# Optimization experiments

Measured on AMD Instinct MI355X. Metric: run time of the kernel, lower is better.

Reference implementation:

```python
import jax, jax.numpy as jnp
import numpy as np

B, N1, N2 = 8, 2048, 2048


def setup_inputs() -> dict:
    key = jax.random.key(0)
    k1, k2 = jax.random.split(key)
    pc_gen = jax.random.normal(k1, (B, N1, 3), dtype=jnp.float32)
    pc_gt = jax.random.normal(k2, (B, N2, 3), dtype=jnp.float32)
    return {"pc_gen": pc_gen, "pc_gt": pc_gt}


def _approx_match(d2, n, m):
    """Faithful JAX port of Fan et al. approxmatch.cu iterative OT matching.
    d2: [B, n, m] squared pairwise distances. Returns match matrix [B, n, m]."""
    b = d2.shape[0]
    factorl = max(n, m) / n  # row capacity
    factorr = max(n, m) / m  # column capacity
    remainl0 = jnp.full((b, n), factorl, dtype=d2.dtype)
    remainr0 = jnp.full((b, m), factorr, dtype=d2.dtype)
    match0 = jnp.zeros_like(d2)
    # levels: j = 7 .. -1 -> -4^j, then final pass with level = 0 (j == -2 case)
    levels = jnp.asarray([-(4.0 ** j) for j in range(7, -2, -1)] + [0.0],
                         dtype=d2.dtype)

    def step(carry, level):
        match, remainl, remainr = carry
        w = jnp.exp(level * d2) * remainr[:, None, :]            # [b,n,m]
        w = w * (remainl / (w.sum(-1) + 1e-9))[:, :, None]       # row-normalize, scale by remainl
        colsum = w.sum(1)                                        # [b,m]
        ratio = jnp.minimum(remainr / (colsum + 1e-9), 1.0)      # column saturation ratio
        w = w * ratio[:, None, :]
        match = match + w
        remainl = jnp.maximum(remainl - w.sum(-1), 0.0)
        remainr = jnp.maximum(remainr - colsum * ratio, 0.0)
        return (match, remainl, remainr), None

    (match, _, _), _ = jax.lax.scan(step, (match0, remainl0, remainr0), levels)
    return match


def reference(pc_gen, pc_gt):
    n, m = pc_gen.shape[1], pc_gt.shape[1]
    diff = pc_gen[:, :, None, :] - pc_gt[:, None, :, :]          # [B,n,m,3]
    d2 = jnp.sum(diff * diff, axis=-1)                           # [B,n,m]
    match = jax.lax.stop_gradient(_approx_match(d2, n, m))
    # matchcost: sum of match-weighted Euclidean distances, per batch
    dist = jnp.sum(match * jnp.sqrt(jnp.maximum(d2, 1e-20)), axis=(1, 2))  # [B]
    emd_loss = (dist / n).mean()
    return emd_loss
```

## Files before the change

kernel.cpp:

```cpp
#include <hip/hip_runtime.h>
#include <math.h>

#define BATCH 8
#define NPTS 2048
#define MPTS 2048
#define TPB 256
#define RPB 16
#define KC 8
#define RPR 2
#define NRND (RPB/RPR)
#define CHUNKS (NPTS/RPB)
#define NBLK (BATCH*CHUNKS)

__device__ float g_remainl[BATCH*NPTS];
__device__ float g_s[BATCH*NPTS];
__device__ float g_rbuf[2][BATCH*MPTS];
__device__ float g_cbuf[3][BATCH*MPTS];
__device__ float g_cost;

#if __has_builtin(__builtin_amdgcn_exp2f)
#define EXP2(x) __builtin_amdgcn_exp2f(x)
#else
#define EXP2(x) exp2f(x)
#endif
#if __has_builtin(__builtin_amdgcn_sqrtf)
#define FSQRT(x) __builtin_amdgcn_sqrtf(x)
#else
#define FSQRT(x) sqrtf(x)
#endif
#if __has_builtin(__builtin_amdgcn_rcpf)
#define RCP(x) __builtin_amdgcn_rcpf(x)
#else
#define RCP(x) (1.0f/(x))
#endif

#define D2(rd, k) fmaf(rd.x, cx[k], fmaf(rd.y, cy[k],                      \
                   fmaf(rd.z, cz[k], rd.w + rc2[k])))

__global__ __launch_bounds__(256) void k_init() {
  const int i = blockIdx.x*256 + threadIdx.x;
  g_cbuf[0][i] = 0.f;
  g_cbuf[1][i] = 0.f;
  g_rbuf[0][i] = 1.f;
  if (i == 0) g_cost = 0.f;
}

__global__ __launch_bounds__(TPB) void k_a0(const float* __restrict__ gen,
                                            const float* __restrict__ gt,
                                            float c1) {
  const int blk = blockIdx.x, b = blk >> 7, chunk = blk & (CHUNKS-1);
  const int t = threadIdx.x, wave = t >> 6, lane = t & 63;
  const int rowbase = b*NPTS + chunk*RPB;
  __shared__ float4 rowdat[RPB];
  __shared__ float2 red[2][4];
  __shared__ float  cred[4];
  float cx[KC], cy[KC], cz[KC], rc2[KC];
  #pragma unroll
  for (int k = 0; k < KC; ++k) {
    const int gi = (b*MPTS + t + TPB*k)*3;
    cx[k] = gt[gi]; cy[k] = gt[gi+1]; cz[k] = gt[gi+2];
    rc2[k] = cx[k]*cx[k] + cy[k]*cy[k] + cz[k]*cz[k];
  }
  if (t < RPB) {
    const int gi = (rowbase + t)*3;
    const float px = gen[gi], py = gen[gi+1], pz = gen[gi+2];
    rowdat[t] = make_float4(-2.f*px, -2.f*py, -2.f*pz, px*px+py*py+pz*pz);
    g_remainl[rowbase + t] = 1.0f;
  }
  __syncthreads();
  float colacc[KC];
  #pragma unroll
  for (int k = 0; k < KC; ++k) colacc[k] = 0.f;
  #pragma unroll 1
  for (int rr = 0; rr < NRND; ++rr) {
    const int buf = rr & 1;
    const float4 rd0 = rowdat[RPR*rr+0];
    const float4 rd1 = rowdat[RPR*rr+1];
    float w0[KC], w1[KC];
    float s1a = 0.f, s1b = 0.f;
    #pragma unroll
    for (int k = 0; k < KC; ++k) {
      const float ea = EXP2(c1*D2(rd0, k));
      const float eb = EXP2(c1*D2(rd1, k));
      w0[k] = ea; s1a += ea;
      w1[k] = eb; s1b += eb;
    }
    #pragma unroll
    for (int off = 1; off < 64; off <<= 1) {
      s1a += __shfl_xor(s1a, off);
      s1b += __shfl_xor(s1b, off);
    }
    if (lane == 0) red[buf][wave] = make_float2(s1a, s1b);
    __syncthreads();
    const float2 v0 = red[buf][0], v1 = red[buf][1];
    const float2 v2 = red[buf][2], v3 = red[buf][3];
    const float scn0 = RCP(v0.x+v1.x+v2.x+v3.x + 1e-9f);
    const float scn1 = RCP(v0.y+v1.y+v2.y+v3.y + 1e-9f);
    if (t == 0) {
      g_s[rowbase + RPR*rr + 0] = scn0;
      g_s[rowbase + RPR*rr + 1] = scn1;
    }
    #pragma unroll
    for (int k = 0; k < KC; ++k)
      colacc[k] = fmaf(w0[k], scn0, fmaf(w1[k], scn1, colacc[k]));
  }
  #pragma unroll
  for (int k = 0; k < KC; ++k)
    atomicAdd(&g_cbuf[0][b*MPTS + t + TPB*k], colacc[k]);
  (void)cred;
}

template<bool LAST>
__global__ __launch_bounds__(TPB) void k_ca(const float* __restrict__ gen,
                                            const float* __restrict__ gt,
                                            float c1, float cq, int l) {
  const int blk = blockIdx.x, b = blk >> 7, chunk = blk & (CHUNKS-1);
  const int t = threadIdx.x, wave = t >> 6, lane = t & 63;
  const int rowbase = b*NPTS + chunk*RPB;
  const float* __restrict__ cs_in = g_cbuf[l % 3];
  float* __restrict__ cs_out  = g_cbuf[(l+1) % 3];
  float* __restrict__ cs_zero = g_cbuf[(l+2) % 3];
  const float* __restrict__ rr_in = g_rbuf[l & 1];
  float* __restrict__ rr_out = g_rbuf[(l+1) & 1];
  __shared__ float4 rowdat[RPB];
  __shared__ float  sc_s[RPB], rl_s[RPB];
  __shared__ float4 red[2][4];
  __shared__ float  cred[4];
  float cx[KC], cy[KC], cz[KC], rc2[KC], pp[KC], rrn[KC];
  #pragma unroll
  for (int k = 0; k < KC; ++k) {
    const int m = b*MPTS + t + TPB*k;
    const int gi = m*3;
    cx[k] = gt[gi]; cy[k] = gt[gi+1]; cz[k] = gt[gi+2];
    rc2[k] = cx[k]*cx[k] + cy[k]*cy[k] + cz[k]*cz[k];
    const float cs = cs_in[m], rrv = rr_in[m];
    const float ratio = fminf(rrv / (cs + 1e-9f), 1.0f);
    pp[k]  = rrv*ratio;
    rrn[k] = fmaxf(rrv - cs*ratio, 0.0f);
    if (chunk == 0) { rr_out[m] = rrn[k]; cs_zero[m] = 0.0f; }
  }
  if (t < RPB) {
    const int gi = (rowbase + t)*3;
    const float px = gen[gi], py = gen[gi+1], pz = gen[gi+2];
    rowdat[t] = make_float4(-2.f*px, -2.f*py, -2.f*pz, px*px+py*py+pz*pz);
    sc_s[t] = g_s[rowbase + t];
    rl_s[t] = g_remainl[rowbase + t];
  }
  __syncthreads();
  float colacc[KC];
  #pragma unroll
  for (int k = 0; k < KC; ++k) colacc[k] = 0.f;
  float costacc = 0.f;
  #pragma unroll 1
  for (int rr = 0; rr < NRND; ++rr) {
    const int buf = rr & 1;
    const int r0 = RPR*rr, r1 = r0 + 1;
    const float4 rd0 = rowdat[r0];
    const float4 rd1 = rowdat[r1];
    float w0[KC], w1[KC];
    float s1a = 0.f, rsa = 0.f, s2a = 0.f;
    float s1b = 0.f, rsb = 0.f, s2b = 0.f;
    #pragma unroll
    for (int k = 0; k < KC; ++k) {
      {
        const float d2 = D2(rd0, k);
        float e1, wq;
        if (LAST) { e1 = EXP2(c1*d2); wq = rrn[k]; }
        else { const float eq = EXP2(cq*d2); const float e2 = eq*eq;
               e1 = e2*e2; wq = eq*rrn[k]; }
        w0[k] = wq; rsa += wq;
        const float u = e1*pp[k];
        s1a += u;
        s2a = fmaf(u, FSQRT(fmaxf(d2, 1e-20f)), s2a);
      }
      {
        const float d2 = D2(rd1, k);
        float e1, wq;
        if (LAST) { e1 = EXP2(c1*d2); wq = rrn[k]; }
        else { const float eq = EXP2(cq*d2); const float e2 = eq*eq;
               e1 = e2*e2; wq = eq*rrn[k]; }
        w1[k] = wq; rsb += wq;
        const float u = e1*pp[k];
        s1b += u;
        s2b = fmaf(u, FSQRT(fmaxf(d2, 1e-20f)), s2b);
      }
    }
    costacc = fmaf(sc_s[r0], s2a, costacc);
    costacc = fmaf(sc_s[r1], s2b, costacc);
    #pragma unroll
    for (int off = 1; off < 64; off <<= 1) {
      s1a += __shfl_xor(s1a, off); rsa += __shfl_xor(rsa, off);
      s1b += __shfl_xor(s1b, off); rsb += __shfl_xor(rsb, off);
    }
    if (lane == 0) red[buf][wave] = make_float4(s1a, rsa, s1b, rsb);
    __syncthreads();
    const float4 v0 = red[buf][0], v1 = red[buf][1];
    const float4 v2 = red[buf][2], v3 = red[buf][3];
    const float s1t0 = v0.x+v1.x+v2.x+v3.x;
    const float rst0 = v0.y+v1.y+v2.y+v3.y;
    const float s1t1 = v0.z+v1.z+v2.z+v3.z;
    const float rst1 = v0.w+v1.w+v2.w+v3.w;
    const float rl0 = fmaxf(rl_s[r0] - sc_s[r0]*s1t0, 0.0f);
    const float rl1 = fmaxf(rl_s[r1] - sc_s[r1]*s1t1, 0.0f);
    const float scn0 = rl0 * RCP(rst0 + 1e-9f);
    const float scn1 = rl1 * RCP(rst1 + 1e-9f);
    if (t == 0) {
      g_remainl[rowbase + r0] = rl0;
      g_remainl[rowbase + r1] = rl1;
      g_s[rowbase + r0] = scn0;
      g_s[rowbase + r1] = scn1;
    }
    #pragma unroll
    for (int k = 0; k < KC; ++k)
      colacc[k] = fmaf(w0[k], scn0, fmaf(w1[k], scn1, colacc[k]));
  }
  #pragma unroll
  for (int k = 0; k < KC; ++k)
    atomicAdd(&cs_out[b*MPTS + t + TPB*k], colacc[k]);
  #pragma unroll
  for (int off = 1; off < 64; off <<= 1) costacc += __shfl_xor(costacc, off);
  if (lane == 0) cred[wave] = costacc;
  __syncthreads();
  if (t == 0)
    atomicAdd(&g_cost, cred[0] + cred[1] + cred[2] + cred[3]);
}

__global__ __launch_bounds__(TPB) void k_c_last(const float* __restrict__ gen,
                                                const float* __restrict__ gt) {
  const int blk = blockIdx.x, b = blk >> 7, chunk = blk & (CHUNKS-1);
  const int t = threadIdx.x, wave = t >> 6, lane = t & 63;
  const int rowbase = b*NPTS + chunk*RPB;
  const float* __restrict__ cs_in = g_cbuf[0];
  const float* __restrict__ rr_in = g_rbuf[1];
  __shared__ float4 rowdat[RPB];
  __shared__ float  sc_s[RPB];
  __shared__ float  cred[4];
  float cx[KC], cy[KC], cz[KC], rc2[KC], pp[KC];
  #pragma unroll
  for (int k = 0; k < KC; ++k) {
    const int m = b*MPTS + t + TPB*k;
    const int gi = m*3;
    cx[k] = gt[gi]; cy[k] = gt[gi+1]; cz[k] = gt[gi+2];
    rc2[k] = cx[k]*cx[k] + cy[k]*cy[k] + cz[k]*cz[k];
    const float cs = cs_in[m], rrv = rr_in[m];
    const float ratio = fminf(rrv / (cs + 1e-9f), 1.0f);
    pp[k] = rrv*ratio;
  }
  if (t < RPB) {
    const int gi = (rowbase + t)*3;
    const float px = gen[gi], py = gen[gi+1], pz = gen[gi+2];
    rowdat[t] = make_float4(-2.f*px, -2.f*py, -2.f*pz, px*px+py*py+pz*pz);
    sc_s[t] = g_s[rowbase + t];
  }
  __syncthreads();
  float costacc = 0.f;
  #pragma unroll 1
  for (int r = 0; r < RPB; ++r) {
    const float4 rd = rowdat[r];
    float s2 = 0.f;
    #pragma unroll
    for (int k = 0; k < KC; ++k)
      s2 = fmaf(pp[k], FSQRT(fmaxf(D2(rd, k), 1e-20f)), s2);
    costacc = fmaf(sc_s[r], s2, costacc);
  }
  #pragma unroll
  for (int off = 1; off < 64; off <<= 1) costacc += __shfl_xor(costacc, off);
  if (lane == 0) cred[wave] = costacc;
  __syncthreads();
  if (t == 0)
    atomicAdd(&g_cost, cred[0] + cred[1] + cred[2] + cred[3]);
}

__global__ void k_final(float* __restrict__ out) {
  out[0] = g_cost * (1.0f / (float)(BATCH*NPTS));
}

extern "C" void kernel_launch(void* const* d_in, const int* in_sizes, int n_in,
                              void* d_out, int out_size, void* d_ws, size_t ws_size,
                              hipStream_t stream) {
  const float* gen = (const float*)d_in[0];
  const float* gt  = (const float*)d_in[1];
  float* out = (float*)d_out;

  const double L[10] = {-16384.0, -4096.0, -1024.0, -256.0, -64.0,
                        -16.0, -4.0, -1.0, -0.25, 0.0};
  float c[10];
  for (int i = 0; i < 10; ++i) c[i] = (float)(L[i] * 1.4426950408889634);

  k_init<<<64, 256, 0, stream>>>();
  k_a0<<<NBLK, TPB, 0, stream>>>(gen, gt, c[0]);
  for (int l = 0; l < 8; ++l)
    k_ca<false><<<NBLK, TPB, 0, stream>>>(gen, gt, c[l], c[l+1], l);
  k_ca<true><<<NBLK, TPB, 0, stream>>>(gen, gt, c[8], 0.f, 8);
  k_c_last<<<NBLK, TPB, 0, stream>>>(gen, gt);
  k_final<<<1, 1, 0, stream>>>(out);
}
```

Before: 366.7 us.

## Halve rows per block, precompute packed float4 points, use DPP wave reductions

Rows per block drop from 16 to 8, doubling the grid to 2048 blocks so more blocks are resident per GPU, at the cost of twice as many column atomics and twice the per-block reloading of column state. Point coordinates and squared norms are computed once in the init kernel into float4 device buffers, so each later kernel does a single vector load instead of three strided loads plus recomputation. Wave reductions use DPP row operations for the first steps in place of a full shuffle ladder, which lowers reduction latency per round.

```diff
diff --git a/kernel.cpp b/kernel.cpp
--- a/kernel.cpp
+++ b/kernel.cpp
@@ -5,18 +5,20 @@
 #define NPTS 2048
 #define MPTS 2048
 #define TPB 256
-#define RPB 16
+#define RPB 8
 #define KC 8
 #define RPR 2
 #define NRND (RPB/RPR)
 #define CHUNKS (NPTS/RPB)
 #define NBLK (BATCH*CHUNKS)
 
-__device__ float g_remainl[BATCH*NPTS];
-__device__ float g_s[BATCH*NPTS];
-__device__ float g_rbuf[2][BATCH*MPTS];
-__device__ float g_cbuf[3][BATCH*MPTS];
-__device__ float g_cost;
+__device__ float  g_remainl[BATCH*NPTS];
+__device__ float  g_s[BATCH*NPTS];
+__device__ float  g_rbuf[2][BATCH*MPTS];
+__device__ float  g_cbuf[3][BATCH*MPTS];
+__device__ float4 g_gt4[BATCH*MPTS];
+__device__ float4 g_gen4[BATCH*NPTS];
+__device__ float  g_cost;
 
 #if __has_builtin(__builtin_amdgcn_exp2f)
 #define EXP2(x) __builtin_amdgcn_exp2f(x)
@@ -34,37 +36,71 @@
 #define RCP(x) (1.0f/(x))
 #endif
 
+template<int CTRL>
+__device__ __forceinline__ float dpp_add(float x) {
+  const int y = __builtin_amdgcn_update_dpp(0, __float_as_int(x),
+                                            CTRL, 0xF, 0xF, true);
+  return x + __int_as_float(y);
+}
+__device__ __forceinline__ void wsum_step4(float& a, float& b, float& c, float& d) {
+  a = dpp_add<0xB1>(a);  b = dpp_add<0xB1>(b);
+  c = dpp_add<0xB1>(c);  d = dpp_add<0xB1>(d);
+  a = dpp_add<0x4E>(a);  b = dpp_add<0x4E>(b);
+  c = dpp_add<0x4E>(c);  d = dpp_add<0x4E>(d);
+  a = dpp_add<0x141>(a); b = dpp_add<0x141>(b);
+  c = dpp_add<0x141>(c); d = dpp_add<0x141>(d);
+  a = dpp_add<0x140>(a); b = dpp_add<0x140>(b);
+  c = dpp_add<0x140>(c); d = dpp_add<0x140>(d);
+  a += __shfl_xor(a, 16); b += __shfl_xor(b, 16);
+  c += __shfl_xor(c, 16); d += __shfl_xor(d, 16);
+  a += __shfl_xor(a, 32); b += __shfl_xor(b, 32);
+  c += __shfl_xor(c, 32); d += __shfl_xor(d, 32);
+}
+__device__ __forceinline__ void wsum_step2(float& a, float& b) {
+  a = dpp_add<0xB1>(a);  b = dpp_add<0xB1>(b);
+  a = dpp_add<0x4E>(a);  b = dpp_add<0x4E>(b);
+  a = dpp_add<0x141>(a); b = dpp_add<0x141>(b);
+  a = dpp_add<0x140>(a); b = dpp_add<0x140>(b);
+  a += __shfl_xor(a, 16); b += __shfl_xor(b, 16);
+  a += __shfl_xor(a, 32); b += __shfl_xor(b, 32);
+}
+__device__ __forceinline__ float wsum_step1(float a) {
+  a = dpp_add<0xB1>(a); a = dpp_add<0x4E>(a);
+  a = dpp_add<0x141>(a); a = dpp_add<0x140>(a);
+  a += __shfl_xor(a, 16); a += __shfl_xor(a, 32);
+  return a;
+}
+
 #define D2(rd, k) fmaf(rd.x, cx[k], fmaf(rd.y, cy[k],                      \
                    fmaf(rd.z, cz[k], rd.w + rc2[k])))
 
-__global__ __launch_bounds__(256) void k_init() {
+__global__ __launch_bounds__(256) void k_init(const float* __restrict__ gen,
+                                              const float* __restrict__ gt) {
   const int i = blockIdx.x*256 + threadIdx.x;
   g_cbuf[0][i] = 0.f;
   g_cbuf[1][i] = 0.f;
   g_rbuf[0][i] = 1.f;
+  const float tx = gt[i*3], ty = gt[i*3+1], tz = gt[i*3+2];
+  g_gt4[i] = make_float4(tx, ty, tz, tx*tx + ty*ty + tz*tz);
+  const float px = gen[i*3], py = gen[i*3+1], pz = gen[i*3+2];
+  g_gen4[i] = make_float4(-2.f*px, -2.f*py, -2.f*pz, px*px + py*py + pz*pz);
   if (i == 0) g_cost = 0.f;
 }
 
-__global__ __launch_bounds__(TPB) void k_a0(const float* __restrict__ gen,
-                                            const float* __restrict__ gt,
-                                            float c1) {
-  const int blk = blockIdx.x, b = blk >> 7, chunk = blk & (CHUNKS-1);
+__global__ __launch_bounds__(TPB) void k_a0(float c1) {
+  const int blk = blockIdx.x, b = blk >> 8, chunk = blk & (CHUNKS-1);
   const int t = threadIdx.x, wave = t >> 6, lane = t & 63;
   const int rowbase = b*NPTS + chunk*RPB;
   __shared__ float4 rowdat[RPB];
   __shared__ float2 red[2][4];
-  __shared__ float  cred[4];
   float cx[KC], cy[KC], cz[KC], rc2[KC];
   #pragma unroll
   for (int k = 0; k < KC; ++k) {
-    const int gi = (b*MPTS + t + TPB*k)*3;
-    cx[k] = gt[gi]; cy[k] = gt[gi+1]; cz[k] = gt[gi+2];
-    rc2[k] = cx[k]*cx[k] + cy[k]*cy[k] + cz[k]*cz[k];
+    const float4 q = g_gt4[b*MPTS + t + TPB*k];
+    cx[k] = q.x; cy[k] = q.y; cz[k] = q.z; rc2[k] = q.w;
   }
   if (t < RPB) {
-    const int gi = (rowbase + t)*3;
-    const float px = gen[gi], py = gen[gi+1], pz = gen[gi+2];
-    rowdat[t] = make_float4(-2.f*px, -2.f*py, -2.f*pz, px*px+py*py+pz*pz);
+    rowdat[t] = g_gen4[rowbase + t];
     g_remainl[rowbase + t] = 1.0f;
   }
   __syncthreads();
@@ -73,7 +109,6 @@
   for (int k = 0; k < KC; ++k) colacc[k] = 0.f;
   #pragma unroll 1
   for (int rr = 0; rr < NRND; ++rr) {
-    const int buf = rr & 1;
     const float4 rd0 = rowdat[RPR*rr+0];
     const float4 rd1 = rowdat[RPR*rr+1];
     float w0[KC], w1[KC];
@@ -85,15 +120,11 @@
       w0[k] = ea; s1a += ea;
       w1[k] = eb; s1b += eb;
     }
-    #pragma unroll
-    for (int off = 1; off < 64; off <<= 1) {
-      s1a += __shfl_xor(s1a, off);
-      s1b += __shfl_xor(s1b, off);
-    }
-    if (lane == 0) red[buf][wave] = make_float2(s1a, s1b);
+    wsum_step2(s1a, s1b);
+    if (lane == 0) red[rr&1][wave] = make_float2(s1a, s1b);
     __syncthreads();
-    const float2 v0 = red[buf][0], v1 = red[buf][1];
-    const float2 v2 = red[buf][2], v3 = red[buf][3];
+    const float2 v0 = red[rr&1][0], v1 = red[rr&1][1];
+    const float2 v2 = red[rr&1][2], v3 = red[rr&1][3];
     const float scn0 = RCP(v0.x+v1.x+v2.x+v3.x + 1e-9f);
     const float scn1 = RCP(v0.y+v1.y+v2.y+v3.y + 1e-9f);
     if (t == 0) {
@@ -107,14 +138,11 @@
   #pragma unroll
   for (int k = 0; k < KC; ++k)
     atomicAdd(&g_cbuf[0][b*MPTS + t + TPB*k], colacc[k]);
-  (void)cred;
 }
 
 template<bool LAST>
-__global__ __launch_bounds__(TPB) void k_ca(const float* __restrict__ gen,
-                                            const float* __restrict__ gt,
-                                            float c1, float cq, int l) {
-  const int blk = blockIdx.x, b = blk >> 7, chunk = blk & (CHUNKS-1);
+__global__ __launch_bounds__(TPB) void k_ca(float c1, float cq, int l) {
+  const int blk = blockIdx.x, b = blk >> 8, chunk = blk & (CHUNKS-1);
   const int t = threadIdx.x, wave = t >> 6, lane = t & 63;
   const int rowbase = b*NPTS + chunk*RPB;
   const float* __restrict__ cs_in = g_cbuf[l % 3];
@@ -130,9 +158,8 @@
   #pragma unroll
   for (int k = 0; k < KC; ++k) {
     const int m = b*MPTS + t + TPB*k;
-    const int gi = m*3;
-    cx[k] = gt[gi]; cy[k] = gt[gi+1]; cz[k] = gt[gi+2];
-    rc2[k] = cx[k]*cx[k] + cy[k]*cy[k] + cz[k]*cz[k];
+    const float4 q = g_gt4[m];
+    cx[k] = q.x; cy[k] = q.y; cz[k] = q.z; rc2[k] = q.w;
     const float cs = cs_in[m], rrv = rr_in[m];
     const float ratio = fminf(rrv / (cs + 1e-9f), 1.0f);
     pp[k]  = rrv*ratio;
@@ -140,9 +167,7 @@
     if (chunk == 0) { rr_out[m] = rrn[k]; cs_zero[m] = 0.0f; }
   }
   if (t < RPB) {
-    const int gi = (rowbase + t)*3;
-    const float px = gen[gi], py = gen[gi+1], pz = gen[gi+2];
-    rowdat[t] = make_float4(-2.f*px, -2.f*py, -2.f*pz, px*px+py*py+pz*pz);
+    rowdat[t] = g_gen4[rowbase + t];
     sc_s[t] = g_s[rowbase + t];
     rl_s[t] = g_remainl[rowbase + t];
   }
@@ -153,7 +178,6 @@
   float costacc = 0.f;
   #pragma unroll 1
   for (int rr = 0; rr < NRND; ++rr) {
-    const int buf = rr & 1;
     const int r0 = RPR*rr, r1 = r0 + 1;
     const float4 rd0 = rowdat[r0];
     const float4 rd1 = rowdat[r1];
@@ -187,15 +211,11 @@
     }
     costacc = fmaf(sc_s[r0], s2a, costacc);
     costacc = fmaf(sc_s[r1], s2b, costacc);
-    #pragma unroll
-    for (int off = 1; off < 64; off <<= 1) {
-      s1a += __shfl_xor(s1a, off); rsa += __shfl_xor(rsa, off);
-      s1b += __shfl_xor(s1b, off); rsb += __shfl_xor(rsb, off);
-    }
-    if (lane == 0) red[buf][wave] = make_float4(s1a, rsa, s1b, rsb);
+    wsum_step4(s1a, rsa, s1b, rsb);
+    if (lane == 0) red[rr&1][wave] = make_float4(s1a, rsa, s1b, rsb);
     __syncthreads();
-    const float4 v0 = red[buf][0], v1 = red[buf][1];
-    const float4 v2 = red[buf][2], v3 = red[buf][3];
+    const float4 v0 = red[rr&1][0], v1 = red[rr&1][1];
+    const float4 v2 = red[rr&1][2], v3 = red[rr&1][3];
     const float s1t0 = v0.x+v1.x+v2.x+v3.x;
     const float rst0 = v0.y+v1.y+v2.y+v3.y;
     const float s1t1 = v0.z+v1.z+v2.z+v3.z;
@@ -217,17 +237,15 @@
   #pragma unroll
   for (int k = 0; k < KC; ++k)
     atomicAdd(&cs_out[b*MPTS + t + TPB*k], colacc[k]);
-  #pragma unroll
-  for (int off = 1; off < 64; off <<= 1) costacc += __shfl_xor(costacc, off);
+  costacc = wsum_step1(costacc);
   if (lane == 0) cred[wave] = costacc;
   __syncthreads();
   if (t == 0)
     atomicAdd(&g_cost, cred[0] + cred[1] + cred[2] + cred[3]);
 }
 
-__global__ __launch_bounds__(TPB) void k_c_last(const float* __restrict__ gen,
-                                                const float* __restrict__ gt) {
-  const int blk = blockIdx.x, b = blk >> 7, chunk = blk & (CHUNKS-1);
+__global__ __launch_bounds__(TPB) void k_c_last() {
+  const int blk = blockIdx.x, b = blk >> 8, chunk = blk & (CHUNKS-1);
   const int t = threadIdx.x, wave = t >> 6, lane = t & 63;
   const int rowbase = b*NPTS + chunk*RPB;
   const float* __restrict__ cs_in = g_cbuf[0];
@@ -239,17 +257,14 @@
   #pragma unroll
   for (int k = 0; k < KC; ++k) {
     const int m = b*MPTS + t + TPB*k;
-    const int gi = m*3;
-    cx[k] = gt[gi]; cy[k] = gt[gi+1]; cz[k] = gt[gi+2];
-    rc2[k] = cx[k]*cx[k] + cy[k]*cy[k] + cz[k]*cz[k];
+    const float4 q = g_gt4[m];
+    cx[k] = q.x; cy[k] = q.y; cz[k] = q.z; rc2[k] = q.w;
     const float cs = cs_in[m], rrv = rr_in[m];
     const float ratio = fminf(rrv / (cs + 1e-9f), 1.0f);
     pp[k] = rrv*ratio;
   }
   if (t < RPB) {
-    const int gi = (rowbase + t)*3;
-    const float px = gen[gi], py = gen[gi+1], pz = gen[gi+2];
-    rowdat[t] = make_float4(-2.f*px, -2.f*py, -2.f*pz, px*px+py*py+pz*pz);
+    rowdat[t] = g_gen4[rowbase + t];
     sc_s[t] = g_s[rowbase + t];
   }
   __syncthreads();
@@ -263,8 +278,7 @@
       s2 = fmaf(pp[k], FSQRT(fmaxf(D2(rd, k), 1e-20f)), s2);
     costacc = fmaf(sc_s[r], s2, costacc);
   }
-  #pragma unroll
-  for (int off = 1; off < 64; off <<= 1) costacc += __shfl_xor(costacc, off);
+  costacc = wsum_step1(costacc);
   if (lane == 0) cred[wave] = costacc;
   __syncthreads();
   if (t == 0)
@@ -287,11 +301,11 @@
   float c[10];
   for (int i = 0; i < 10; ++i) c[i] = (float)(L[i] * 1.4426950408889634);
 
-  k_init<<<64, 256, 0, stream>>>();
-  k_a0<<<NBLK, TPB, 0, stream>>>(gen, gt, c[0]);
+  k_init<<<64, 256, 0, stream>>>(gen, gt);
+  k_a0<<<NBLK, TPB, 0, stream>>>(c[0]);
   for (int l = 0; l < 8; ++l)
-    k_ca<false><<<NBLK, TPB, 0, stream>>>(gen, gt, c[l], c[l+1], l);
-  k_ca<true><<<NBLK, TPB, 0, stream>>>(gen, gt, c[8], 0.f, 8);
-  k_c_last<<<NBLK, TPB, 0, stream>>>(gen, gt);
+    k_ca<false><<<NBLK, TPB, 0, stream>>>(c[l], c[l+1], l);
+  k_ca<true><<<NBLK, TPB, 0, stream>>>(c[8], 0.f, 8);
+  k_c_last<<<NBLK, TPB, 0, stream>>>();
   k_final<<<1, 1, 0, stream>>>(out);
 }
```

Measured after the change: 487.0 us. 32.8% more time.
